# Performance work log

Hardware: AMD Instinct MI355X
Metric: run time of the kernel (lower is better)

## Reference

```python
import jax, jax.numpy as jnp
import numpy as np


def setup_inputs() -> dict:
    key = jax.random.key(0)
    k1, k2, k3 = jax.random.split(key, 3)
    B, D, R, O = 8192, 2048, 16, 64
    # small init scale so the 2048-step matrix chain product stays numerically sane
    inputs = jax.random.normal(k1, (B, D), dtype=jnp.float32) * 0.05
    # cores near identity (glorot-scale perturbation) to avoid chain blow-up/collapse
    cores = jnp.eye(R, dtype=jnp.float32)[None] + jax.random.normal(k2, (D, R, R), dtype=jnp.float32) * (1.0 / R)
    projection = jax.random.normal(k3, (R, O), dtype=jnp.float32) * (1.0 / np.sqrt(R))
    bias = jnp.zeros((O,), dtype=jnp.float32)
    return {"inputs": inputs, "cores": cores, "projection": projection, "bias": bias}


def reference(inputs, cores, projection, bias):
    # inputs: (B, D); cores: (D, R, R); projection: (R, O); bias: (O,)
    B = inputs.shape[0]
    R = cores.shape[-1]
    boundary0 = jnp.ones((B, R), dtype=inputs.dtype)  # MPS boundary vector

    x_t = inputs.T  # (D, B) so scan iterates over features

    def step(boundary, xs):
        core, x = xs  # core: (R, R), x: (B,)
        # boundary <- (boundary @ core) scaled by the feature value (A^i[x_i])
        boundary = jnp.matmul(boundary, core) * x[:, None]
        return boundary, None

    boundary, _ = jax.lax.scan(step, boundary0, (cores, x_t))
    out = jnp.matmul(boundary, projection) + bias  # (B, O)
    return out
```

## Files before the change

### kernel.cpp

```cpp
#include <hip/hip_runtime.h>
#include <math.h>


#define DFEAT 2048
#define R 16
#define NR2 256
#define OUTD 64
#define CHUNK 64
#define NCHUNK (DFEAT / CHUNK)
#define MAGIC 0x7E57C0DE

__device__ __forceinline__ float4 rowmul(const float* Arow, const float* B,
                                         int c0) {
    float4 acc = {0.f, 0.f, 0.f, 0.f};
    const float4* a4 = (const float4*)Arow;
#pragma unroll
    for (int kk = 0; kk < 4; ++kk) {
        const float4 av = a4[kk];
        const float4 b0 = *(const float4*)&B[(4 * kk + 0) * 16 + c0];
        const float4 b1 = *(const float4*)&B[(4 * kk + 1) * 16 + c0];
        const float4 b2 = *(const float4*)&B[(4 * kk + 2) * 16 + c0];
        const float4 b3 = *(const float4*)&B[(4 * kk + 3) * 16 + c0];
        acc.x = fmaf(av.x, b0.x, fmaf(av.y, b1.x, fmaf(av.z, b2.x, fmaf(av.w, b3.x, acc.x))));
        acc.y = fmaf(av.x, b0.y, fmaf(av.y, b1.y, fmaf(av.z, b2.y, fmaf(av.w, b3.y, acc.y))));
        acc.z = fmaf(av.x, b0.z, fmaf(av.y, b1.z, fmaf(av.z, b2.z, fmaf(av.w, b3.z, acc.z))));
        acc.w = fmaf(av.x, b0.w, fmaf(av.y, b1.w, fmaf(av.z, b2.w, fmaf(av.w, b3.w, acc.w))));
    }
    return acc;
}

__global__ __launch_bounds__(256) void mps_chain(const float* __restrict__ cores,
                                                 const float* __restrict__ proj,
                                                 float* __restrict__ partials,
                                                 int* __restrict__ flags,
                                                 float* __restrict__ pE) {
    __shared__ __align__(16) float Cs[CHUNK * NR2];
    __shared__ __align__(16) float Aw[4][2][NR2];
    __shared__ __align__(16) float F[2][NR2];
    __shared__ __align__(16) float Pt[NCHUNK * NR2];
    const int tid  = threadIdx.x;
    const int wave = tid >> 6, lane = tid & 63;
    const int ri = lane >> 2;
    const int c0 = (lane & 3) << 2;
    const size_t d0 = (size_t)blockIdx.x * CHUNK;

    const float4* g4 = (const float4*)(cores + d0 * NR2);
    float4* s4 = (float4*)&Cs[0];
#pragma unroll
    for (int q = 0; q < 16; ++q)
        s4[q * 256 + tid] = g4[q * 256 + tid];
    __syncthreads();

    *(float4*)&Aw[wave][0][ri * 16 + c0] =
        *(const float4*)&Cs[(16 * wave) * NR2 + ri * 16 + c0];
    int cur = 0;
    for (int t = 1; t < 16; ++t) {
        float4 r = rowmul(&Aw[wave][cur][ri * 16],
                          &Cs[(16 * wave + t) * NR2], c0);
        *(float4*)&Aw[wave][cur ^ 1][ri * 16 + c0] = r;
        cur ^= 1;
    }
    __syncthreads();

    if (wave == 0) {
        *(float4*)&F[0][ri * 16 + c0] =
            *(const float4*)&Aw[0][1][ri * 16 + c0];
        int cc = 0;
        for (int w = 1; w < 4; ++w) {
            float4 r = rowmul(&F[cc][ri * 16], &Aw[w][1][0], c0);
            *(float4*)&F[cc ^ 1][ri * 16 + c0] = r;
            cc ^= 1;
        }
    }
    __syncthreads();
    const int i = tid >> 4, j = tid & 15;
    const float v = F[1][tid];

    if (blockIdx.x != 0) {
        partials[blockIdx.x * NR2 + tid] = v;
        __syncthreads();
        if (tid == 0)
            __hip_atomic_store(&flags[blockIdx.x], MAGIC,
                               __ATOMIC_RELEASE, __HIP_MEMORY_SCOPE_AGENT);
        return;
    }

    Pt[0 * 256 + j * 16 + i] = v;

    {
        const int f = 1 + (tid % (NCHUNK - 1));
        while (__hip_atomic_load(&flags[f], __ATOMIC_ACQUIRE,
                                 __HIP_MEMORY_SCOPE_AGENT) != MAGIC) { }
    }
    __syncthreads();

#pragma unroll
    for (int q = 0; q < 8; ++q) {
        const int idx = q * 256 + tid;
        if (idx < (NCHUNK - 1) * 64) {
            float4 p4 = ((const float4*)(partials + NR2))[idx];
            const int flat = idx * 4;
            const int gg = (flat >> 8) + 1;
            const int e = flat & 255;
            const int k = e >> 4, j0 = e & 15;
            Pt[gg * 256 + (j0 + 0) * 16 + k] = p4.x;
            Pt[gg * 256 + (j0 + 1) * 16 + k] = p4.y;
            Pt[gg * 256 + (j0 + 2) * 16 + k] = p4.z;
            Pt[gg * 256 + (j0 + 3) * 16 + k] = p4.w;
        }
    }
    __syncthreads();

    if (tid < 64) {
        const int jj = tid & 15, q = tid >> 4;
        float w = 1.f;
        int E = 0;
        for (int gg = 0; gg < NCHUNK; ++gg) {
            const float4 pr = *(const float4*)&Pt[gg * 256 + jj * 16 + 4 * q];
            float s;
            s = __shfl(w, 4 * q + 0) * pr.x;
            s = fmaf(__shfl(w, 4 * q + 1), pr.y, s);
            s = fmaf(__shfl(w, 4 * q + 2), pr.z, s);
            s = fmaf(__shfl(w, 4 * q + 3), pr.w, s);
            s += __shfl_xor(s, 16);
            s += __shfl_xor(s, 32);
            w = s;
            if ((gg & 7) == 7) {
                float m = fabsf(w);
#pragma unroll
                for (int off = 1; off <= 8; off <<= 1)
                    m = fmaxf(m, __shfl_xor(m, off));
                if (m > 0.f) {
                    int e = 0;
                    (void)frexpf(m, &e);
                    w = ldexpf(w, -e);
                    E += e;
                }
            }
        }
        float p = 0.f;
#pragma unroll
        for (int k = 0; k < R; ++k)
            p = fmaf(__shfl(w, k), proj[k * OUTD + tid], p);
        pE[tid] = p;
        if (tid == 0) ((int*)pE)[OUTD] = E;
    }
}

__global__ __launch_bounds__(256) void mps_rows(const float* __restrict__ x,
                                                const float* __restrict__ pE,
                                                const float* __restrict__ bias,
                                                float* __restrict__ out,
                                                int B) {
    const int gtid = blockIdx.x * 256 + threadIdx.x;
    const int row  = gtid >> 6;
    const int lane = threadIdx.x & 63;
    if (row >= B) return;

    const float4* xr = (const float4*)(x + (size_t)row * DFEAT);
    float prod = 1.f;
#pragma unroll
    for (int it = 0; it < DFEAT / (64 * 4); ++it) {
        float4 v = xr[it * 64 + lane];
        prod *= (v.x * v.y) * (v.z * v.w);
    }
#pragma unroll
    for (int off = 32; off > 0; off >>= 1)
        prod *= __shfl_xor(prod, off);

    const float pv = pE[lane];
    const int   E  = ((const int*)pE)[OUTD];
    out[(size_t)row * OUTD + lane] = ldexpf(pv * prod, E) + bias[lane];
}

extern "C" void kernel_launch(void* const* d_in, const int* in_sizes, int n_in,
                              void* d_out, int out_size, void* d_ws, size_t ws_size,
                              hipStream_t stream) {
    const float* inputs = (const float*)d_in[0];
    const float* cores  = (const float*)d_in[1];
    const float* proj   = (const float*)d_in[2];
    const float* bias   = (const float*)d_in[3];
    float* out = (float*)d_out;

    float* partials = (float*)d_ws;
    float* pE    = partials + NCHUNK * NR2;
    int*   flags = (int*)(pE + 68);

    const int B = in_sizes[0] / DFEAT;

    mps_chain<<<NCHUNK, 256, 0, stream>>>(cores, proj, partials, flags, pE);
    mps_rows<<<(B * 64 + 255) / 256, 256, 0, stream>>>(inputs, pE, bias, out, B);
}
```

Baseline: 107.4 us.

## Fuse row-product reduction into chain kernel to overlap it with the serial core chain

The per-row product over the inputs now runs in extra blocks of the chain kernel and is written to a small buffer, so the large input read can overlap with the latency-bound core-chain blocks. The second kernel only scales and writes the output. Cores are streamed from global memory with a one-step register prefetch instead of being staged whole in shared memory, and the partial-matrix transpose buffer is processed in four rounds of eight. Together these shrink shared memory use. The cost is an extra buffer write and read and more synchronisation rounds in the reduction block, which still spins on flags while sharing the GPU with the row blocks.

```diff
diff --git a/kernel.cpp b/kernel.cpp
--- a/kernel.cpp
+++ b/kernel.cpp
@@ -29,34 +29,52 @@
     return acc;
 }
 
-__global__ __launch_bounds__(256) void mps_chain(const float* __restrict__ cores,
+__global__ __launch_bounds__(256) void mps_fused(const float* __restrict__ cores,
                                                  const float* __restrict__ proj,
+                                                 const float* __restrict__ x,
+                                                 float* __restrict__ prodbuf,
                                                  float* __restrict__ partials,
                                                  int* __restrict__ flags,
-                                                 float* __restrict__ pE) {
-    __shared__ __align__(16) float Cs[CHUNK * NR2];
+                                                 float* __restrict__ pE,
+                                                 int B) {
+    __shared__ __align__(16) float Bb[4][2][NR2];
     __shared__ __align__(16) float Aw[4][2][NR2];
     __shared__ __align__(16) float F[2][NR2];
-    __shared__ __align__(16) float Pt[NCHUNK * NR2];
+    __shared__ __align__(16) float Pt[8 * NR2];
+
     const int tid  = threadIdx.x;
     const int wave = tid >> 6, lane = tid & 63;
+
+    if (blockIdx.x >= NCHUNK) {
+        const int row = (blockIdx.x - NCHUNK) * 4 + wave;
+        if (row >= B) return;
+        const float4* xr = (const float4*)(x + (size_t)row * DFEAT);
+        float prod = 1.f;
+#pragma unroll
+        for (int it = 0; it < DFEAT / (64 * 4); ++it) {
+            float4 v = xr[it * 64 + lane];
+            prod *= (v.x * v.y) * (v.z * v.w);
+        }
+#pragma unroll
+        for (int off = 32; off > 0; off >>= 1)
+            prod *= __shfl_xor(prod, off);
+        if (lane == 0) prodbuf[row] = prod;
+        return;
+    }
+
     const int ri = lane >> 2;
     const int c0 = (lane & 3) << 2;
     const size_t d0 = (size_t)blockIdx.x * CHUNK;
 
-    const float4* g4 = (const float4*)(cores + d0 * NR2);
-    float4* s4 = (float4*)&Cs[0];
-#pragma unroll
-    for (int q = 0; q < 16; ++q)
-        s4[q * 256 + tid] = g4[q * 256 + tid];
-    __syncthreads();
-
-    *(float4*)&Aw[wave][0][ri * 16 + c0] =
-        *(const float4*)&Cs[(16 * wave) * NR2 + ri * 16 + c0];
+    const float* gw = cores + (d0 + 16 * wave) * NR2;
+    *(float4*)&Aw[wave][0][lane * 4] = *(const float4*)&gw[lane * 4];
+    float4 nxt = *(const float4*)&gw[NR2 + lane * 4];
     int cur = 0;
     for (int t = 1; t < 16; ++t) {
-        float4 r = rowmul(&Aw[wave][cur][ri * 16],
-                          &Cs[(16 * wave + t) * NR2], c0);
+        *(float4*)&Bb[wave][t & 1][lane * 4] = nxt;
+        if (t < 15)
+            nxt = *(const float4*)&gw[(size_t)(t + 1) * NR2 + lane * 4];
+        float4 r = rowmul(&Aw[wave][cur][ri * 16], &Bb[wave][t & 1][0], c0);
         *(float4*)&Aw[wave][cur ^ 1][ri * 16 + c0] = r;
         cur ^= 1;
     }
@@ -94,50 +112,54 @@
     }
     __syncthreads();
 
-#pragma unroll
-    for (int q = 0; q < 8; ++q) {
-        const int idx = q * 256 + tid;
-        if (idx < (NCHUNK - 1) * 64) {
-            float4 p4 = ((const float4*)(partials + NR2))[idx];
+    float w = 1.f;
+    int E = 0;
+    for (int rr = 0; rr < 4; ++rr) {
+#pragma unroll
+        for (int q = 0; q < 2; ++q) {
+            const int idx = q * 256 + tid;
             const int flat = idx * 4;
-            const int gg = (flat >> 8) + 1;
-            const int e = flat & 255;
-            const int k = e >> 4, j0 = e & 15;
-            Pt[gg * 256 + (j0 + 0) * 16 + k] = p4.x;
-            Pt[gg * 256 + (j0 + 1) * 16 + k] = p4.y;
-            Pt[gg * 256 + (j0 + 2) * 16 + k] = p4.z;
-            Pt[gg * 256 + (j0 + 3) * 16 + k] = p4.w;
-        }
-    }
-    __syncthreads();
+            const int s = flat >> 8;
+            if (rr > 0 || s > 0) {
+                float4 p4 =
+                    ((const float4*)(partials + (size_t)(8 * rr) * NR2))[idx];
+                const int e = flat & 255;
+                const int k = e >> 4, j0 = e & 15;
+                Pt[s * 256 + (j0 + 0) * 16 + k] = p4.x;
+                Pt[s * 256 + (j0 + 1) * 16 + k] = p4.y;
+                Pt[s * 256 + (j0 + 2) * 16 + k] = p4.z;
+                Pt[s * 256 + (j0 + 3) * 16 + k] = p4.w;
+            }
+        }
+        __syncthreads();
+        if (tid < 64) {
+            const int jj = tid & 15, q = tid >> 4;
+            for (int s = 0; s < 8; ++s) {
+                const float4 pr = *(const float4*)&Pt[s * 256 + jj * 16 + 4 * q];
+                float sum;
+                sum = __shfl(w, 4 * q + 0) * pr.x;
+                sum = fmaf(__shfl(w, 4 * q + 1), pr.y, sum);
+                sum = fmaf(__shfl(w, 4 * q + 2), pr.z, sum);
+                sum = fmaf(__shfl(w, 4 * q + 3), pr.w, sum);
+                sum += __shfl_xor(sum, 16);
+                sum += __shfl_xor(sum, 32);
+                w = sum;
+            }
+            float m = fabsf(w);
+#pragma unroll
+            for (int off = 1; off <= 8; off <<= 1)
+                m = fmaxf(m, __shfl_xor(m, off));
+            if (m > 0.f) {
+                int e2 = 0;
+                (void)frexpf(m, &e2);
+                w = ldexpf(w, -e2);
+                E += e2;
+            }
+        }
+        __syncthreads();
+    }
 
     if (tid < 64) {
-        const int jj = tid & 15, q = tid >> 4;
-        float w = 1.f;
-        int E = 0;
-        for (int gg = 0; gg < NCHUNK; ++gg) {
-            const float4 pr = *(const float4*)&Pt[gg * 256 + jj * 16 + 4 * q];
-            float s;
-            s = __shfl(w, 4 * q + 0) * pr.x;
-            s = fmaf(__shfl(w, 4 * q + 1), pr.y, s);
-            s = fmaf(__shfl(w, 4 * q + 2), pr.z, s);
-            s = fmaf(__shfl(w, 4 * q + 3), pr.w, s);
-            s += __shfl_xor(s, 16);
-            s += __shfl_xor(s, 32);
-            w = s;
-            if ((gg & 7) == 7) {
-                float m = fabsf(w);
-#pragma unroll
-                for (int off = 1; off <= 8; off <<= 1)
-                    m = fmaxf(m, __shfl_xor(m, off));
-                if (m > 0.f) {
-                    int e = 0;
-                    (void)frexpf(m, &e);
-                    w = ldexpf(w, -e);
-                    E += e;
-                }
-            }
-        }
         float p = 0.f;
 #pragma unroll
         for (int k = 0; k < R; ++k)
@@ -147,30 +169,18 @@
     }
 }
 
-__global__ __launch_bounds__(256) void mps_rows(const float* __restrict__ x,
-                                                const float* __restrict__ pE,
-                                                const float* __restrict__ bias,
-                                                float* __restrict__ out,
-                                                int B) {
+__global__ __launch_bounds__(256) void mps_scale(const float* __restrict__ prodbuf,
+                                                 const float* __restrict__ pE,
+                                                 const float* __restrict__ bias,
+                                                 float* __restrict__ out,
+                                                 int B) {
     const int gtid = blockIdx.x * 256 + threadIdx.x;
     const int row  = gtid >> 6;
     const int lane = threadIdx.x & 63;
     if (row >= B) return;
-
-    const float4* xr = (const float4*)(x + (size_t)row * DFEAT);
-    float prod = 1.f;
-#pragma unroll
-    for (int it = 0; it < DFEAT / (64 * 4); ++it) {
-        float4 v = xr[it * 64 + lane];
-        prod *= (v.x * v.y) * (v.z * v.w);
-    }
-#pragma unroll
-    for (int off = 32; off > 0; off >>= 1)
-        prod *= __shfl_xor(prod, off);
-
     const float pv = pE[lane];
     const int   E  = ((const int*)pE)[OUTD];
-    out[(size_t)row * OUTD + lane] = ldexpf(pv * prod, E) + bias[lane];
+    out[(size_t)row * OUTD + lane] = ldexpf(pv * prodbuf[row], E) + bias[lane];
 }
 
 extern "C" void kernel_launch(void* const* d_in, const int* in_sizes, int n_in,
@@ -182,12 +192,17 @@
     const float* bias   = (const float*)d_in[3];
     float* out = (float*)d_out;
 
-    float* partials = (float*)d_ws;
+    const int B = in_sizes[0] / DFEAT;
+
+    float* prodbuf  = (float*)d_ws;
+    float* partials = prodbuf + B;
     float* pE    = partials + NCHUNK * NR2;
     int*   flags = (int*)(pE + 68);
 
-    const int B = in_sizes[0] / DFEAT;
-
-    mps_chain<<<NCHUNK, 256, 0, stream>>>(cores, proj, partials, flags, pE);
-    mps_rows<<<(B * 64 + 255) / 256, 256, 0, stream>>>(inputs, pE, bias, out, B);
-}
+    const int rowBlocks = (B + 3) / 4;
+    mps_fused<<<NCHUNK + rowBlocks, 256, 0, stream>>>(cores, proj, inputs,
+                                                      prodbuf, partials, flags,
+                                                      pE, B);
+    mps_scale<<<(B * 64 + 255) / 256, 256, 0, stream>>>(prodbuf, pE, bias,
+                                                        out, B);
+}
```

Result: faster. 105.2 us (-2.0%).
